# Optimization experiments

Measured on AMD Instinct MI355X. Metric: run time of the kernel, lower is better.

## Reference

```python
import jax, jax.numpy as jnp
import numpy as np

B, C, H, W = 4, 256, 64, 64
CK = C // 8  # query/key channels per OUT_RATIO=8


def setup_inputs() -> dict:
    key = jax.random.key(0)
    ks = jax.random.split(key, 8)
    s_in = 1.0 / np.sqrt(C)
    return {
        "x": jax.random.normal(ks[0], (B, C, H, W), dtype=jnp.float32),
        "Wq": jax.random.uniform(ks[1], (CK, C), jnp.float32, -s_in, s_in),
        "bq": jax.random.uniform(ks[2], (CK,), jnp.float32, -s_in, s_in),
        "Wk": jax.random.uniform(ks[3], (CK, C), jnp.float32, -s_in, s_in),
        "bk": jax.random.uniform(ks[4], (CK,), jnp.float32, -s_in, s_in),
        "Wv": jax.random.uniform(ks[5], (C, C), jnp.float32, -s_in, s_in),
        "bv": jax.random.uniform(ks[6], (C,), jnp.float32, -s_in, s_in),
        "gamma": jnp.zeros((1,), dtype=jnp.float32),
    }


def reference(x, Wq, bq, Wk, bk, Wv, bv, gamma):
    b, c, h, w = x.shape
    n = h * w
    xf = x.reshape(b, c, n)  # [B, C, N]
    # 1x1 convs are channel matmuls
    q = jnp.einsum('oc,bcn->bno', Wq, xf) + bq  # [B, N, CK]
    k = jnp.einsum('oc,bcn->bon', Wk, xf) + bk[None, :, None]  # [B, CK, N]
    v = jnp.einsum('oc,bcn->bon', Wv, xf) + bv[None, :, None]  # [B, C, N]
    energy = jnp.einsum('bno,bom->bnm', q, k)  # [B, N, N], unscaled
    attn = jax.nn.softmax(energy, axis=-1)
    out = jnp.einsum('bcm,bnm->bcn', v, attn)  # [B, C, N]
    out = out.reshape(b, c, h, w)
    return gamma[0] * out + x
```

## Files before the change

### kernel.cpp

```cpp
#include <hip/hip_runtime.h>
#include <math.h>


#define BB 4
#define CC 256
#define NN 4096
#define CKK 32

typedef __attribute__((ext_vector_type(4))) float f32x4;
typedef __attribute__((ext_vector_type(16))) float f32x16;
typedef __attribute__((ext_vector_type(8))) short short8;
typedef __attribute__((ext_vector_type(4))) short short4v;

static __device__ __forceinline__ ushort f2bf(float f) {
    union { float f; unsigned u; } v; v.f = f;
    unsigned r = v.u + 0x7FFFu + ((v.u >> 16) & 1u);
    return (ushort)(r >> 16);
}
static __device__ __forceinline__ float bf2f(ushort h) {
    union { unsigned u; float f; } v; v.u = ((unsigned)h) << 16;
    return v.f;
}
static __device__ __forceinline__ unsigned pack2(float lo, float hi) {
    return ((unsigned)f2bf(hi) << 16) | (unsigned)f2bf(lo);
}

__global__ __launch_bounds__(256) void pack_w_kernel(
    const float* __restrict__ Wq, const float* __restrict__ bq,
    const float* __restrict__ Wk, const float* __restrict__ bk,
    const float* __restrict__ Wv, const float* __restrict__ bv,
    ushort* __restrict__ Wb, float* __restrict__ bias)
{
    const int o = blockIdx.x;
    const int c = threadIdx.x;
    const float* src; float bsc;
    if (o < 32)      { src = Wq + o * CC;        bsc = bq[o]; }
    else if (o < 64) { src = Wk + (o - 32) * CC; bsc = bk[o - 32]; }
    else             { src = Wv + (o - 64) * CC; bsc = bv[o - 64]; }
    Wb[o * CC + c] = f2bf(src[c]);
    if (c == 0) bias[o] = bsc;
}

__global__ __launch_bounds__(256) void xpose_kernel(
    const float* __restrict__ x, ushort* __restrict__ xT)
{
    __shared__ float t[32][33];
    const int b = blockIdx.z, c0 = blockIdx.y * 32, n0 = blockIdx.x * 32;
    const int tid = threadIdx.x;
    #pragma unroll
    for (int i = 0; i < 4; ++i) {
        int idx = tid + i * 256, rr = idx >> 5, nn = idx & 31;
        t[rr][nn] = x[((size_t)b * CC + c0 + rr) * NN + n0 + nn];
    }
    __syncthreads();
    #pragma unroll
    for (int i = 0; i < 4; ++i) {
        int idx = tid + i * 256, rr = idx >> 5, cc = idx & 31;
        xT[((size_t)b * NN + n0 + rr) * CC + c0 + cc] = f2bf(t[cc][rr]);
    }
}

__global__ __launch_bounds__(256) void qkv_mfma_kernel(
    const ushort* __restrict__ Wb, const float* __restrict__ bias,
    const ushort* __restrict__ xT,
    ushort* __restrict__ Q, ushort* __restrict__ Kt, ushort* __restrict__ V)
{
    const int b = blockIdx.y, n0 = blockIdx.x * 64;
    const int tid = threadIdx.x;
    const int w = tid >> 6, lane = tid & 63, l15 = lane & 15, q = lane >> 4;

    f32x4 acc[5][4];
    #pragma unroll
    for (int c5 = 0; c5 < 5; ++c5)
        #pragma unroll
        for (int nc = 0; nc < 4; ++nc) acc[c5][nc] = (f32x4)0.f;

    #pragma unroll
    for (int ks = 0; ks < 8; ++ks) {
        short8 af[5], bf[4];
        #pragma unroll
        for (int c5 = 0; c5 < 5; ++c5)
            af[c5] = *(const short8*)&Wb[(w * 80 + c5 * 16 + l15) * CC + ks * 32 + q * 8];
        #pragma unroll
        for (int nc = 0; nc < 4; ++nc)
            bf[nc] = *(const short8*)&xT[((size_t)b * NN + n0 + nc * 16 + l15) * CC + ks * 32 + q * 8];
        #pragma unroll
        for (int c5 = 0; c5 < 5; ++c5)
            #pragma unroll
            for (int nc = 0; nc < 4; ++nc)
                acc[c5][nc] = __builtin_amdgcn_mfma_f32_16x16x32_bf16(af[c5], bf[nc], acc[c5][nc], 0, 0, 0);
    }

    #pragma unroll
    for (int c5 = 0; c5 < 5; ++c5) {
        const int o0 = w * 80 + c5 * 16;
        float bia[4];
        #pragma unroll
        for (int r = 0; r < 4; ++r) bia[r] = bias[o0 + q * 4 + r];
        if (o0 >= 64) {
            #pragma unroll
            for (int nc = 0; nc < 4; ++nc)
                #pragma unroll
                for (int r = 0; r < 4; ++r)
                    V[((size_t)b * CC + o0 - 64 + q * 4 + r) * NN + n0 + nc * 16 + l15] =
                        f2bf(acc[c5][nc][r] + bia[r]);
        } else {
            ushort* dst = (o0 < 32) ? Q : Kt;
            const int oo = (o0 & 31) + q * 4;
            #pragma unroll
            for (int nc = 0; nc < 4; ++nc) {
                short4v h;
                #pragma unroll
                for (int r = 0; r < 4; ++r) h[r] = (short)f2bf(acc[c5][nc][r] + bia[r]);
                *(short4v*)&dst[((size_t)b * NN + n0 + nc * 16 + l15) * CKK + oo] = h;
            }
        }
    }
}

__global__ __launch_bounds__(256, 2) void attn_mfma_kernel(
    const ushort* __restrict__ Q, const ushort* __restrict__ K,
    const ushort* __restrict__ V,
    ushort* __restrict__ Op, float* __restrict__ Mp, float* __restrict__ Lp,
    int G, int NSEG)
{
    __shared__ __align__(16) ushort vs[2][256][40];

    const int id = blockIdx.x;
    const int xcd = id & 7, ix = id >> 3;
    const int b = xcd >> 1;
    int g, row;
    if (G == 4) { g = ((xcd & 1) << 1) | (ix & 1); row = ix >> 1; }
    else        { g = xcd & 1;                     row = ix; }
    const int n0 = row * 128;

    const int tid = threadIdx.x;
    const int w = tid >> 6, lane = tid & 63;
    const int l31 = lane & 31, h2 = lane >> 5;
    const int n0w = n0 + w * 32;

    const size_t qrow = ((size_t)b * NN + n0w + l31) * CKK;
    short8 qB0 = *(const short8*)&Q[qrow + h2 * 8];
    short8 qB1 = *(const short8*)&Q[qrow + 16 + h2 * 8];

    f32x16 acc[8];
    #pragma unroll
    for (int cb = 0; cb < 8; ++cb) acc[cb] = (f32x16)0.f;
    float m_i = -3.0e38f, l_p = 0.f;

    const size_t kgb = (size_t)b * NN * CKK;
    const size_t vgb = (size_t)b * CC * NN;
    const int m_start = g * NSEG;
    const int NT = NSEG / 32;

    const int srow = tid >> 2, sseg = tid & 3;

    short8 kA0 = *(const short8*)&K[kgb + (size_t)(m_start + l31) * CKK + h2 * 8];
    short8 kA1 = *(const short8*)&K[kgb + (size_t)(m_start + l31) * CKK + 16 + h2 * 8];
    short8 vreg[4];
    #pragma unroll
    for (int i = 0; i < 4; ++i)
        vreg[i] = *(const short8*)&V[vgb + (size_t)(srow + i * 64) * NN + m_start + sseg * 8];
    #pragma unroll
    for (int i = 0; i < 4; ++i)
        *(short8*)&vs[0][srow + i * 64][sseg * 8] = vreg[i];
    __syncthreads();

    int cur = 0;
    for (int mt = 0; mt < NT; ++mt) {
        const bool more = (mt + 1 < NT);
        const int m0n = more ? m_start + (mt + 1) * 32 : m_start;

        f32x16 s = __builtin_amdgcn_mfma_f32_32x32x16_bf16(kA0, qB0, (f32x16)0.f, 0, 0, 0);
        s = __builtin_amdgcn_mfma_f32_32x32x16_bf16(kA1, qB1, s, 0, 0, 0);

        kA0 = *(const short8*)&K[kgb + (size_t)(m0n + l31) * CKK + h2 * 8];
        kA1 = *(const short8*)&K[kgb + (size_t)(m0n + l31) * CKK + 16 + h2 * 8];
        #pragma unroll
        for (int i = 0; i < 4; ++i)
            vreg[i] = *(const short8*)&V[vgb + (size_t)(srow + i * 64) * NN + m0n + sseg * 8];

        float mx01 = fmaxf(s[0], s[1]),   mx23 = fmaxf(s[2], s[3]);
        float mx45 = fmaxf(s[4], s[5]),   mx67 = fmaxf(s[6], s[7]);
        float mx89 = fmaxf(s[8], s[9]),   mxab = fmaxf(s[10], s[11]);
        float mxcd = fmaxf(s[12], s[13]), mxef = fmaxf(s[14], s[15]);
        float mx = fmaxf(fmaxf(fmaxf(mx01, mx23), fmaxf(mx45, mx67)),
                         fmaxf(fmaxf(mx89, mxab), fmaxf(mxcd, mxef)));
        mx = fmaxf(mx, __shfl_xor(mx, 32));
        const bool resc = mx > m_i + 8.f;
        const float mn = resc ? mx : m_i;
        const float al = resc ? __expf(m_i - mx) : 1.f;
        float pp[16];
        #pragma unroll
        for (int r = 0; r < 16; ++r) pp[r] = __expf(s[r] - mn);
        float sum = ((pp[0] + pp[1]) + (pp[2] + pp[3])) + ((pp[4] + pp[5]) + (pp[6] + pp[7]))
                  + ((pp[8] + pp[9]) + (pp[10] + pp[11])) + ((pp[12] + pp[13]) + (pp[14] + pp[15]));
        l_p = l_p * al + sum;
        m_i = mn;
        if (__any(resc)) {
            #pragma unroll
            for (int cb = 0; cb < 8; ++cb) acc[cb] *= al;
        }

        union { unsigned u[8]; short8 v[2]; } P;
        #pragma unroll
        for (int g2 = 0; g2 < 8; ++g2) P.u[g2] = pack2(pp[2 * g2], pp[2 * g2 + 1]);

        __builtin_amdgcn_s_setprio(1);
        #pragma unroll
        for (int cb = 0; cb < 8; ++cb) {
            const ushort* vrow = &vs[cur][cb * 32 + l31][0];
            union { short4v h[2]; short8 v; } A0, A1;
            A0.h[0] = *(const short4v*)&vrow[h2 * 4];
            A0.h[1] = *(const short4v*)&vrow[8 + h2 * 4];
            A1.h[0] = *(const short4v*)&vrow[16 + h2 * 4];
            A1.h[1] = *(const short4v*)&vrow[24 + h2 * 4];
            acc[cb] = __builtin_amdgcn_mfma_f32_32x32x16_bf16(A0.v, P.v[0], acc[cb], 0, 0, 0);
            acc[cb] = __builtin_amdgcn_mfma_f32_32x32x16_bf16(A1.v, P.v[1], acc[cb], 0, 0, 0);
        }
        __builtin_amdgcn_s_setprio(0);

        #pragma unroll
        for (int i = 0; i < 4; ++i)
            *(short8*)&vs[cur ^ 1][srow + i * 64][sseg * 8] = vreg[i];
        __syncthreads();
        cur ^= 1;
    }

    float l = l_p + __shfl_xor(l_p, 32);
    const float linv = 1.f / l;
    if (h2 == 0) {
        const size_t idx = (size_t)(g * BB + b) * NN + n0w + l31;
        Mp[idx] = m_i;
        Lp[idx] = l;
    }
    ushort* ob = Op + (size_t)(g * BB + b) * CC * NN;
    #pragma unroll
    for (int cb = 0; cb < 8; ++cb)
        #pragma unroll
        for (int r = 0; r < 16; ++r) {
            const int c = cb * 32 + (r & 3) + 8 * (r >> 2) + 4 * h2;
            ob[(size_t)c * NN + n0w + l31] = f2bf(acc[cb][r] * linv);
        }
}

template<int G>
__global__ __launch_bounds__(256) void combine_kernel(
    const ushort* __restrict__ Op, const float* __restrict__ Mp,
    const float* __restrict__ Lp, const float* __restrict__ x,
    const float* __restrict__ gamma, float* __restrict__ out)
{
    const int gid = blockIdx.x * 256 + threadIdx.x;
    const int grp   = gid & (NN / 8 - 1);
    const int rowid = gid >> 9;
    const int b = rowid >> 8;
    const int c = rowid & (CC - 1);
    const int n0 = grp * 8;

    f32x4 mp[G][2], lp[G][2];
    #pragma unroll
    for (int g = 0; g < G; ++g) {
        const size_t base = (size_t)(g * BB + b) * NN + n0;
        mp[g][0] = *(const f32x4*)&Mp[base];
        mp[g][1] = *(const f32x4*)&Mp[base + 4];
        lp[g][0] = *(const f32x4*)&Lp[base];
        lp[g][1] = *(const f32x4*)&Lp[base + 4];
    }
    float wgt[G][8];
    #pragma unroll
    for (int h = 0; h < 2; ++h) {
        #pragma unroll
        for (int j = 0; j < 4; ++j) {
            float M = -3.0e38f;
            #pragma unroll
            for (int g = 0; g < G; ++g) M = fmaxf(M, mp[g][h][j]);
            float ws = 0.f;
            #pragma unroll
            for (int g = 0; g < G; ++g) {
                const float wv = lp[g][h][j] * __expf(mp[g][h][j] - M);
                wgt[g][h * 4 + j] = wv;
                ws += wv;
            }
            const float inv = 1.f / ws;
            #pragma unroll
            for (int g = 0; g < G; ++g) wgt[g][h * 4 + j] *= inv;
        }
    }

    short8 opv[G];
    #pragma unroll
    for (int g = 0; g < G; ++g)
        opv[g] = *(const short8*)&Op[((size_t)(g * BB + b) * CC + c) * NN + n0];

    const size_t xbase = ((size_t)b * CC + c) * NN + n0;
    const f32x4 x0 = *(const f32x4*)&x[xbase];
    const f32x4 x1 = *(const f32x4*)&x[xbase + 4];
    const float gm = gamma[0];

    f32x4 o0, o1;
    #pragma unroll
    for (int j = 0; j < 4; ++j) {
        float a = 0.f, bsum = 0.f;
        #pragma unroll
        for (int g = 0; g < G; ++g) {
            a    += wgt[g][j]     * bf2f((ushort)opv[g][j]);
            bsum += wgt[g][4 + j] * bf2f((ushort)opv[g][4 + j]);
        }
        o0[j] = gm * a + x0[j];
        o1[j] = gm * bsum + x1[j];
    }
    *(f32x4*)&out[xbase]     = o0;
    *(f32x4*)&out[xbase + 4] = o1;
}

extern "C" void kernel_launch(void* const* d_in, const int* in_sizes, int n_in,
                              void* d_out, int out_size, void* d_ws, size_t ws_size,
                              hipStream_t stream) {
    const float* x     = (const float*)d_in[0];
    const float* Wq    = (const float*)d_in[1];
    const float* bq    = (const float*)d_in[2];
    const float* Wk    = (const float*)d_in[3];
    const float* bk    = (const float*)d_in[4];
    const float* Wv    = (const float*)d_in[5];
    const float* bv    = (const float*)d_in[6];
    const float* gamma = (const float*)d_in[7];
    float* out = (float*)d_out;

    char* p = (char*)d_ws;
    ushort* Wb   = (ushort*)(p);
    float*  bias = (float*) (p + 163840);
    ushort* xT   = (ushort*)(p + 165120);
    ushort* Qb   = (ushort*)(p + 8553728);
    ushort* Kb   = (ushort*)(p + 9602304);
    ushort* Vc   = (ushort*)(p + 10650880);
    float*  Mpb  = (float*) (p + 19039488);
    float*  Lpb  = (float*) (p + 19301632);
    ushort* Opb  = (ushort*)(p + 19563776);
    const int G = (ws_size >= (size_t)53118208) ? 4 : 2;

    pack_w_kernel<<<dim3(320), 256, 0, stream>>>(Wq, bq, Wk, bk, Wv, bv, Wb, bias);
    xpose_kernel<<<dim3(NN / 32, CC / 32, BB), 256, 0, stream>>>(x, xT);
    qkv_mfma_kernel<<<dim3(NN / 64, BB), 256, 0, stream>>>(Wb, bias, xT, Qb, Kb, Vc);
    attn_mfma_kernel<<<dim3(128 * G), 256, 0, stream>>>(Qb, Kb, Vc, Opb, Mpb, Lpb, G, NN / G);
    const int cblocks = BB * CC * (NN / 8) / 256;
    if (G == 4)
        combine_kernel<4><<<dim3(cblocks), 256, 0, stream>>>(Opb, Mpb, Lpb, x, gamma, out);
    else
        combine_kernel<2><<<dim3(cblocks), 256, 0, stream>>>(Opb, Mpb, Lpb, x, gamma, out);
}
```

Baseline: 99.14 us.

## Fold log2e into Q, use exp2 and hardware bf16 pack, swizzle V LDS layout

Scales Q by log2(e) in the projection so the softmax can use the native exp2 instruction instead of __expf, which multiplies by log2e internally. Replaces the software bf16 rounding in pack2 with the v_cvt_pk_bf16_f32 instruction. Changes the V shared-memory tile from padded rows to a chunked, XOR-swizzled layout with 8-byte accesses to cut LDS bank conflicts and padding. Folding log2e into bf16-rounded Q slightly changes rounding, and the merge step now treats the stored maxima as base-2 values.

```diff
diff --git a/kernel.cpp b/kernel.cpp
--- a/kernel.cpp
+++ b/kernel.cpp
@@ -6,6 +6,7 @@
 #define CC 256
 #define NN 4096
 #define CKK 32
+#define LOG2E 1.44269504f
 
 typedef __attribute__((ext_vector_type(4))) float f32x4;
 typedef __attribute__((ext_vector_type(16))) float f32x16;
@@ -22,8 +23,15 @@
     return v.f;
 }
 static __device__ __forceinline__ unsigned pack2(float lo, float hi) {
-    return ((unsigned)f2bf(hi) << 16) | (unsigned)f2bf(lo);
-}
+    unsigned r;
+    asm("v_cvt_pk_bf16_f32 %0, %1, %2" : "=v"(r) : "v"(lo), "v"(hi));
+    return r;
+}
+static __device__ __forceinline__ float exp2fast(float x) {
+    return __builtin_amdgcn_exp2f(x);
+}
+
+#define VSEL(chunk, c) (((chunk) * 1024) + ((((c) ^ (((chunk) >> 1) << 2))) << 2))
 
 __global__ __launch_bounds__(256) void pack_w_kernel(
     const float* __restrict__ Wq, const float* __restrict__ bq,
@@ -106,12 +114,13 @@
                         f2bf(acc[c5][nc][r] + bia[r]);
         } else {
             ushort* dst = (o0 < 32) ? Q : Kt;
+            const float sc = (o0 < 32) ? LOG2E : 1.0f;
             const int oo = (o0 & 31) + q * 4;
             #pragma unroll
             for (int nc = 0; nc < 4; ++nc) {
                 short4v h;
                 #pragma unroll
-                for (int r = 0; r < 4; ++r) h[r] = (short)f2bf(acc[c5][nc][r] + bia[r]);
+                for (int r = 0; r < 4; ++r) h[r] = (short)f2bf((acc[c5][nc][r] + bia[r]) * sc);
                 *(short4v*)&dst[((size_t)b * NN + n0 + nc * 16 + l15) * CKK + oo] = h;
             }
         }
@@ -124,7 +133,7 @@
     ushort* __restrict__ Op, float* __restrict__ Mp, float* __restrict__ Lp,
     int G, int NSEG)
 {
-    __shared__ __align__(16) ushort vs[2][256][40];
+    __shared__ __align__(16) ushort vs2[2][8192];
 
     const int id = blockIdx.x;
     const int xcd = id & 7, ix = id >> 3;
@@ -157,13 +166,16 @@
 
     short8 kA0 = *(const short8*)&K[kgb + (size_t)(m_start + l31) * CKK + h2 * 8];
     short8 kA1 = *(const short8*)&K[kgb + (size_t)(m_start + l31) * CKK + 16 + h2 * 8];
-    short8 vreg[4];
+    union { short8 v; short4v h[2]; } vr[4];
     #pragma unroll
     for (int i = 0; i < 4; ++i)
-        vreg[i] = *(const short8*)&V[vgb + (size_t)(srow + i * 64) * NN + m_start + sseg * 8];
-    #pragma unroll
-    for (int i = 0; i < 4; ++i)
-        *(short8*)&vs[0][srow + i * 64][sseg * 8] = vreg[i];
+        vr[i].v = *(const short8*)&V[vgb + (size_t)(srow + i * 64) * NN + m_start + sseg * 8];
+    #pragma unroll
+    for (int i = 0; i < 4; ++i) {
+        const int c = srow + i * 64;
+        *(short4v*)&vs2[0][VSEL(2 * sseg,     c)] = vr[i].h[0];
+        *(short4v*)&vs2[0][VSEL(2 * sseg + 1, c)] = vr[i].h[1];
+    }
     __syncthreads();
 
     int cur = 0;
@@ -178,21 +190,20 @@
         kA1 = *(const short8*)&K[kgb + (size_t)(m0n + l31) * CKK + 16 + h2 * 8];
         #pragma unroll
         for (int i = 0; i < 4; ++i)
-            vreg[i] = *(const short8*)&V[vgb + (size_t)(srow + i * 64) * NN + m0n + sseg * 8];
-
-        float mx01 = fmaxf(s[0], s[1]),   mx23 = fmaxf(s[2], s[3]);
-        float mx45 = fmaxf(s[4], s[5]),   mx67 = fmaxf(s[6], s[7]);
-        float mx89 = fmaxf(s[8], s[9]),   mxab = fmaxf(s[10], s[11]);
-        float mxcd = fmaxf(s[12], s[13]), mxef = fmaxf(s[14], s[15]);
-        float mx = fmaxf(fmaxf(fmaxf(mx01, mx23), fmaxf(mx45, mx67)),
-                         fmaxf(fmaxf(mx89, mxab), fmaxf(mxcd, mxef)));
+            vr[i].v = *(const short8*)&V[vgb + (size_t)(srow + i * 64) * NN + m0n + sseg * 8];
+
+        float mx = fmaxf(
+            fmaxf(fmaxf(fmaxf(s[0], s[1]), fmaxf(s[2], s[3])),
+                  fmaxf(fmaxf(s[4], s[5]), fmaxf(s[6], s[7]))),
+            fmaxf(fmaxf(fmaxf(s[8], s[9]), fmaxf(s[10], s[11])),
+                  fmaxf(fmaxf(s[12], s[13]), fmaxf(s[14], s[15]))));
         mx = fmaxf(mx, __shfl_xor(mx, 32));
         const bool resc = mx > m_i + 8.f;
         const float mn = resc ? mx : m_i;
-        const float al = resc ? __expf(m_i - mx) : 1.f;
+        const float al = resc ? exp2fast(m_i - mx) : 1.f;
         float pp[16];
         #pragma unroll
-        for (int r = 0; r < 16; ++r) pp[r] = __expf(s[r] - mn);
+        for (int r = 0; r < 16; ++r) pp[r] = exp2fast(s[r] - mn);
         float sum = ((pp[0] + pp[1]) + (pp[2] + pp[3])) + ((pp[4] + pp[5]) + (pp[6] + pp[7]))
                   + ((pp[8] + pp[9]) + (pp[10] + pp[11])) + ((pp[12] + pp[13]) + (pp[14] + pp[15]));
         l_p = l_p * al + sum;
@@ -209,20 +220,23 @@
         __builtin_amdgcn_s_setprio(1);
         #pragma unroll
         for (int cb = 0; cb < 8; ++cb) {
-            const ushort* vrow = &vs[cur][cb * 32 + l31][0];
+            const int c = cb * 32 + l31;
             union { short4v h[2]; short8 v; } A0, A1;
-            A0.h[0] = *(const short4v*)&vrow[h2 * 4];
-            A0.h[1] = *(const short4v*)&vrow[8 + h2 * 4];
-            A1.h[0] = *(const short4v*)&vrow[16 + h2 * 4];
-            A1.h[1] = *(const short4v*)&vrow[24 + h2 * 4];
+            A0.h[0] = *(const short4v*)&vs2[cur][VSEL(h2,     c)];
+            A0.h[1] = *(const short4v*)&vs2[cur][VSEL(2 + h2, c)];
+            A1.h[0] = *(const short4v*)&vs2[cur][VSEL(4 + h2, c)];
+            A1.h[1] = *(const short4v*)&vs2[cur][VSEL(6 + h2, c)];
             acc[cb] = __builtin_amdgcn_mfma_f32_32x32x16_bf16(A0.v, P.v[0], acc[cb], 0, 0, 0);
             acc[cb] = __builtin_amdgcn_mfma_f32_32x32x16_bf16(A1.v, P.v[1], acc[cb], 0, 0, 0);
         }
         __builtin_amdgcn_s_setprio(0);
 
         #pragma unroll
-        for (int i = 0; i < 4; ++i)
-            *(short8*)&vs[cur ^ 1][srow + i * 64][sseg * 8] = vreg[i];
+        for (int i = 0; i < 4; ++i) {
+            const int c = srow + i * 64;
+            *(short4v*)&vs2[cur ^ 1][VSEL(2 * sseg,     c)] = vr[i].h[0];
+            *(short4v*)&vs2[cur ^ 1][VSEL(2 * sseg + 1, c)] = vr[i].h[1];
+        }
         __syncthreads();
         cur ^= 1;
     }
@@ -277,7 +291,7 @@
             float ws = 0.f;
             #pragma unroll
             for (int g = 0; g < G; ++g) {
-                const float wv = lp[g][h][j] * __expf(mp[g][h][j] - M);
+                const float wv = lp[g][h][j] * exp2fast(mp[g][h][j] - M);
                 wgt[g][h * 4 + j] = wv;
                 ws += wv;
             }
```

After: 97.24 us, median of 2. About the same (-1.9%).
